# Kernel optimization log

Measured on AMD Instinct MI355X. Metric: run time of the kernel, lower is better.

Reference implementation:

```python
import jax, jax.numpy as jnp
import numpy as np

HEADS = 16
DIM_HEAD = 64
LN_EPS = 1e-5
COS_EPS = 1e-8


def setup_inputs() -> dict:
    key = jax.random.key(0)
    ks = jax.random.split(key, 5)
    dim = 1024
    inner = HEADS * DIM_HEAD
    q = jax.random.normal(ks[0], (4, 1024, dim), dtype=jnp.float32)
    k = jax.random.normal(ks[1], (4, 2048, dim), dtype=jnp.float32)
    v = jax.random.normal(ks[2], (4, 2048, dim), dtype=jnp.float32)
    W_in = jax.random.normal(ks[3], (dim, inner), dtype=jnp.float32) * (1.0 / np.sqrt(dim))
    W_out = jax.random.normal(ks[4], (inner, dim), dtype=jnp.float32) * (1.0 / np.sqrt(inner))
    ln_gamma = jnp.ones((dim,), dtype=jnp.float32)
    ln_beta = jnp.zeros((dim,), dtype=jnp.float32)
    b_out = jnp.zeros((dim,), dtype=jnp.float32)
    return {"q": q, "k": k, "v": v, "ln_gamma": ln_gamma, "ln_beta": ln_beta,
            "W_in": W_in, "W_out": W_out, "b_out": b_out}


def _layernorm(x, gamma, beta):
    mu = jnp.mean(x, axis=-1, keepdims=True)
    var = jnp.mean(jnp.square(x - mu), axis=-1, keepdims=True)  # biased, as torch
    return (x - mu) * jax.lax.rsqrt(var + LN_EPS) * gamma + beta


def _project(t, gamma, beta, W_in):
    # LayerNorm -> Linear(no bias) -> split heads: b n (h d) -> b h n d
    x = _layernorm(t, gamma, beta) @ W_in
    b, n, _ = x.shape
    return x.reshape(b, n, HEADS, DIM_HEAD).transpose(0, 2, 1, 3)


def reference(q, k, v, ln_gamma, ln_beta, W_in, W_out, b_out):
    f_q = _project(q, ln_gamma, ln_beta, W_in)  # [b,h,n,d]
    f_k = _project(k, ln_gamma, ln_beta, W_in)  # [b,h,m,d]
    f_v = _project(v, ln_gamma, ln_beta, W_in)  # [b,h,m,d]
    dots = jnp.einsum('bhnd,bhmd->bhnm', f_q, f_k)
    qn = jnp.linalg.norm(f_q, axis=-1, keepdims=True)          # [b,h,n,1]
    kn = jnp.linalg.norm(f_k, axis=-1, keepdims=True)          # [b,h,m,1]
    attn = dots / (qn * kn.transpose(0, 1, 3, 2) + COS_EPS)    # [b,h,n,m]
    out = jnp.einsum('bhnm,bhmd->bhnd', attn, f_v)             # [b,h,n,d]
    b, h, n, d = out.shape
    out = out.transpose(0, 2, 1, 3).reshape(b, n, h * d)       # b n (h d)
    return out @ W_out + b_out
```

## Files before the change

### kernel.cpp

```cpp
#include <hip/hip_runtime.h>

constexpr int BATCH = 4;
constexpr int SEQQ  = 1024;
constexpr int SEQK  = 2048;
constexpr int DIM   = 1024;
constexpr int NH    = 16;
constexpr int DH    = 64;
constexpr int RQ    = BATCH * SEQQ;
constexpr int RK    = BATCH * SEQK;
constexpr int RTOT  = RQ + 2 * RK;
constexpr int BH    = BATCH * NH;
constexpr int NSLC  = 8;
constexpr float LN_EPS = 1e-5f;

typedef _Float16 f16;
typedef __attribute__((ext_vector_type(8))) _Float16 f16x8;
typedef __attribute__((ext_vector_type(4))) float f32x4;

__device__ __forceinline__ void async16(const void* g, void* l) {
  __builtin_amdgcn_global_load_lds(
      (const __attribute__((address_space(1))) void*)g,
      (__attribute__((address_space(3))) void*)l, 16, 0, 0);
}

__global__ void __launch_bounds__(256) ln_to_f16(
    const float* __restrict__ q, const float* __restrict__ k,
    const float* __restrict__ v, const float* __restrict__ gamma,
    const float* __restrict__ beta, f16* __restrict__ a_h) {
  const int row = blockIdx.x * 4 + (threadIdx.x >> 6);
  const int lane = threadIdx.x & 63;
  const float* src;
  if (row < RQ)            src = q + (size_t)row * DIM;
  else if (row < RQ + RK)  src = k + (size_t)(row - RQ) * DIM;
  else                     src = v + (size_t)(row - RQ - RK) * DIM;
  float4 x[4];
  float s = 0.f, s2 = 0.f;
#pragma unroll
  for (int c = 0; c < 4; c++) {
    x[c] = ((const float4*)src)[c * 64 + lane];
    s  += x[c].x + x[c].y + x[c].z + x[c].w;
    s2 += x[c].x * x[c].x + x[c].y * x[c].y + x[c].z * x[c].z + x[c].w * x[c].w;
  }
#pragma unroll
  for (int off = 1; off < 64; off <<= 1) {
    s  += __shfl_xor(s, off);
    s2 += __shfl_xor(s2, off);
  }
  const float mu = s / DIM;
  const float rs = rsqrtf(s2 / DIM - mu * mu + LN_EPS);
#pragma unroll
  for (int c = 0; c < 4; c++) {
    float4 g = ((const float4*)gamma)[c * 64 + lane];
    float4 b = ((const float4*)beta)[c * 64 + lane];
    union { f16 h[4]; uint2 u; } o;
    o.h[0] = (f16)((x[c].x - mu) * rs * g.x + b.x);
    o.h[1] = (f16)((x[c].y - mu) * rs * g.y + b.y);
    o.h[2] = (f16)((x[c].z - mu) * rs * g.z + b.z);
    o.h[3] = (f16)((x[c].w - mu) * rs * g.w + b.w);
    ((uint2*)(a_h + (size_t)row * DIM))[c * 64 + lane] = o.u;
  }
}

__global__ void __launch_bounds__(256) transpose_f16(
    const float* __restrict__ W0, const float* __restrict__ W1,
    f16* __restrict__ T0, f16* __restrict__ T1) {
  const float* W = blockIdx.z ? W1 : W0;
  f16* T = blockIdx.z ? T1 : T0;
  __shared__ float tile[32][33];
  int tx = threadIdx.x & 31, ty = threadIdx.x >> 5;
  int k0 = blockIdx.x * 32, n0 = blockIdx.y * 32;
#pragma unroll
  for (int i = 0; i < 4; i++)
    tile[ty + 8 * i][tx] = W[(size_t)(k0 + ty + 8 * i) * DIM + n0 + tx];
  __syncthreads();
#pragma unroll
  for (int i = 0; i < 4; i++)
    T[(size_t)(n0 + ty + 8 * i) * DIM + k0 + tx] = (f16)tile[tx][ty + 8 * i];
}

template <int MT, bool OUT_F16, bool NORMS, bool BIAS, bool PERB>
__global__ void __launch_bounds__(256) mfma_gemm(
    const f16* __restrict__ A, const f16* __restrict__ Bt,
    void* __restrict__ Cout, const float* __restrict__ bias) {
  constexpr int JT = (MT == 128) ? 4 : 2;
  __shared__ f16 As[2][MT * 32];
  __shared__ f16 Bs[2][128 * 32];
  const int t = threadIdx.x;
  const int wid = t >> 6;
  const int lane = t & 63;
  const int row0 = blockIdx.x * MT;
  const int col0 = blockIdx.y * 128;
  const int wm = (MT == 128) ? (wid >> 1) * 64 : 0;
  const int wn = (MT == 128) ? (wid & 1) * 64 : wid * 32;

  const f16* BtB = PERB ? Bt + (size_t)(row0 >> 10) * DIM * DIM : Bt;

  const int rB = 32 * wid + (lane >> 2);
  const int qB = ((lane & 3) - ((rB >> 1) & 3)) & 3;
  const f16* gB = BtB + (size_t)(col0 + rB) * DIM + qB * 8;
  f16* lB0 = Bs[0] + 32 * wid * 32;
  f16* lB1 = Bs[1] + 32 * wid * 32;
  const int rA = (MT == 128 ? 32 : 16) * wid + (lane >> 2);
  const int qA = ((lane & 3) - ((rA >> 1) & 3)) & 3;
  const f16* gA = A + (size_t)(row0 + rA) * DIM + qA * 8;
  f16* lA0 = As[0] + (MT == 128 ? 32 : 16) * wid * 32;
  f16* lA1 = As[1] + (MT == 128 ? 32 : 16) * wid * 32;

  f32x4 acc[4][JT];
#pragma unroll
  for (int i = 0; i < 4; i++)
#pragma unroll
    for (int j = 0; j < JT; j++) acc[i][j] = (f32x4){0.f, 0.f, 0.f, 0.f};

  const int mrow = lane & 15;
  const int kq_p = (((lane >> 4) + ((lane >> 1) & 3)) & 3) * 8;

  for (int kt = 0; kt < DIM / 64; ++kt) {
    if (kt) __syncthreads();
    const int ko = kt * 64;
    async16(gA + ko,      lA0);
    if (MT == 128) async16(gA + ko + 16 * DIM, lA0 + 512);
    async16(gB + ko,      lB0);
    async16(gB + ko + 16 * DIM, lB0 + 512);
    async16(gA + ko + 32, lA1);
    if (MT == 128) async16(gA + ko + 32 + 16 * DIM, lA1 + 512);
    async16(gB + ko + 32, lB1);
    async16(gB + ko + 32 + 16 * DIM, lB1 + 512);
    __syncthreads();

#pragma unroll
    for (int h = 0; h < 2; ++h) {
      f16x8 af[4], bf[JT];
#pragma unroll
      for (int i = 0; i < 4; i++)
        af[i] = *(const f16x8*)(As[h] + (wm + i * 16 + mrow) * 32 + kq_p);
#pragma unroll
      for (int j = 0; j < JT; j++)
        bf[j] = *(const f16x8*)(Bs[h] + (wn + j * 16 + mrow) * 32 + kq_p);
#pragma unroll
      for (int i = 0; i < 4; i++)
#pragma unroll
        for (int j = 0; j < JT; j++)
          acc[i][j] = __builtin_amdgcn_mfma_f32_16x16x32_f16(af[i], bf[j], acc[i][j], 0, 0, 0);
    }
  }

  if (NORMS && MT == 128) {
    if (row0 < RQ + RK) {
      float sums[4][4];
#pragma unroll
      for (int i = 0; i < 4; i++)
#pragma unroll
        for (int r = 0; r < 4; r++) {
          float s = 0.f;
#pragma unroll
          for (int j = 0; j < JT; j++) s += acc[i][j][r] * acc[i][j][r];
          sums[i][r] = s;
        }
#pragma unroll
      for (int off = 1; off < 16; off <<= 1)
#pragma unroll
        for (int i = 0; i < 4; i++)
#pragma unroll
          for (int r = 0; r < 4; r++)
            sums[i][r] += __shfl_xor(sums[i][r], off);
#pragma unroll
      for (int i = 0; i < 4; i++)
#pragma unroll
        for (int r = 0; r < 4; r++) {
          const float inv = rsqrtf(sums[i][r]);
#pragma unroll
          for (int j = 0; j < JT; j++) acc[i][j][r] *= inv;
        }
    }
  }

  const int ccol = lane & 15;
  const int crow = (lane >> 4) * 4;
  if (OUT_F16) {
    f16* C = (f16*)Cout;
#pragma unroll
    for (int j = 0; j < JT; j++) {
      const int col = col0 + wn + j * 16 + ccol;
#pragma unroll
      for (int i = 0; i < 4; i++) {
        f16* Cp = C + (size_t)(row0 + wm + i * 16 + crow) * DIM + col;
#pragma unroll
        for (int r = 0; r < 4; r++) Cp[(size_t)r * DIM] = (f16)acc[i][j][r];
      }
    }
  } else {
    float* C = (float*)Cout;
#pragma unroll
    for (int j = 0; j < JT; j++) {
      const int col = col0 + wn + j * 16 + ccol;
      float bv = BIAS ? bias[col] : 0.f;
#pragma unroll
      for (int i = 0; i < 4; i++) {
        float* Cp = C + (size_t)(row0 + wm + i * 16 + crow) * DIM + col;
#pragma unroll
        for (int r = 0; r < 4; r++) Cp[(size_t)r * DIM] = acc[i][j][r] + bv;
      }
    }
  }
}

__global__ void __launch_bounds__(256) s_kernel(
    const f16* __restrict__ f, float* __restrict__ S4) {
  const int bh = blockIdx.x;
  const int b = bh >> 4, h = bh & 15;
  const int mbase = blockIdx.y * (SEQK / NSLC);
  const int t = threadIdx.x;
  __shared__ float ks[32][68];
  __shared__ float vs[32][68];
  const int lm   = t >> 3;
  const int lseg = (t & 7) * 8;
  const int d1 = (t & 15) * 4;
  const int d2 = (t >> 4) * 4;
  float acc[4][4] = {{0.f}};
  const f16* fk_base = f + ((size_t)RQ + (size_t)b * SEQK) * DIM + h * DH;
  const f16* fv_base = f + ((size_t)RQ + RK + (size_t)b * SEQK) * DIM + h * DH;

  int m = mbase + lm;
  f16x8 kv = *(const f16x8*)(fk_base + (size_t)m * DIM + lseg);
  f16x8 vv = *(const f16x8*)(fv_base + (size_t)m * DIM + lseg);

  constexpr int SUBS = SEQK / NSLC / 32;
  for (int sub = 0; sub < SUBS; ++sub) {
    __syncthreads();
#pragma unroll
    for (int e = 0; e < 8; e++) {
      ks[lm][lseg + e] = (float)kv[e];
      vs[lm][lseg + e] = (float)vv[e];
    }
    __syncthreads();
    if (sub + 1 < SUBS) {
      m = mbase + (sub + 1) * 32 + lm;
      kv = *(const f16x8*)(fk_base + (size_t)m * DIM + lseg);
      vv = *(const f16x8*)(fv_base + (size_t)m * DIM + lseg);
    }
#pragma unroll
    for (int mm = 0; mm < 32; ++mm) {
      float4 kk = *(const float4*)&ks[mm][d1];
      float4 vv2 = *(const float4*)&vs[mm][d2];
      acc[0][0] = fmaf(kk.x, vv2.x, acc[0][0]);
      acc[0][1] = fmaf(kk.x, vv2.y, acc[0][1]);
      acc[0][2] = fmaf(kk.x, vv2.z, acc[0][2]);
      acc[0][3] = fmaf(kk.x, vv2.w, acc[0][3]);
      acc[1][0] = fmaf(kk.y, vv2.x, acc[1][0]);
      acc[1][1] = fmaf(kk.y, vv2.y, acc[1][1]);
      acc[1][2] = fmaf(kk.y, vv2.z, acc[1][2]);
      acc[1][3] = fmaf(kk.y, vv2.w, acc[1][3]);
      acc[2][0] = fmaf(kk.z, vv2.x, acc[2][0]);
      acc[2][1] = fmaf(kk.z, vv2.y, acc[2][1]);
      acc[2][2] = fmaf(kk.z, vv2.z, acc[2][2]);
      acc[2][3] = fmaf(kk.z, vv2.w, acc[2][3]);
      acc[3][0] = fmaf(kk.w, vv2.x, acc[3][0]);
      acc[3][1] = fmaf(kk.w, vv2.y, acc[3][1]);
      acc[3][2] = fmaf(kk.w, vv2.z, acc[3][2]);
      acc[3][3] = fmaf(kk.w, vv2.w, acc[3][3]);
    }
  }
  float* Sp = S4 + ((size_t)blockIdx.y * BH + bh) * DH * DH;
#pragma unroll
  for (int i = 0; i < 4; i++)
#pragma unroll
    for (int j = 0; j < 4; j++)
      Sp[(d1 + i) * DH + (d2 + j)] = acc[i][j];
}

__global__ void __launch_bounds__(256) s_reduce(
    const float* __restrict__ S4, f16* __restrict__ Sh) {
  const int bh = blockIdx.x;
  const int t = threadIdx.x;
  const size_t base = (size_t)bh * DH * DH + t * 16;
  constexpr size_t STR = (size_t)BH * DH * DH;
#pragma unroll
  for (int c = 0; c < 4; c++) {
    float4 s = {0.f, 0.f, 0.f, 0.f};
#pragma unroll
    for (int p = 0; p < NSLC; p++) {
      float4 sp = *(const float4*)(S4 + base + p * STR + 4 * c);
      s.x += sp.x; s.y += sp.y; s.z += sp.z; s.w += sp.w;
    }
    union { f16 h[4]; uint2 u; } o;
    o.h[0] = (f16)s.x; o.h[1] = (f16)s.y; o.h[2] = (f16)s.z; o.h[3] = (f16)s.w;
    *(uint2*)(Sh + base + 4 * c) = o.u;
  }
}

__global__ void __launch_bounds__(256) m_build(
    const f16* __restrict__ wt_out, const f16* __restrict__ Sh,
    f16* __restrict__ Mt) {
  const int n0 = blockIdx.x * 128;
  const int bh = blockIdx.y;
  const int b = bh >> 4, h = bh & 15;
  __shared__ f16 As[128 * 64];
  __shared__ f16 Bs[64 * 64];
  const int t = threadIdx.x;
  const int wid = t >> 6, lane = t & 63;

  const f16* gA = wt_out + (size_t)(n0 + 32 * wid + (lane >> 3)) * DIM
                  + 64 * h + (lane & 7) * 8;
  f16* lA = As + 32 * wid * 64;
  const f16* gB = Sh + (size_t)bh * DH * DH + (16 * wid + (lane >> 3)) * 64
                  + (lane & 7) * 8;
  f16* lB = Bs + 16 * wid * 64;
#pragma unroll
  for (int o = 0; o < 4; o++) async16(gA + (size_t)(8 * o) * DIM, lA + 8 * o * 64);
  async16(gB, lB);
  async16(gB + 8 * 64, lB + 8 * 64);
  __syncthreads();

  const int wm = (wid >> 1) * 64;
  const int wn = (wid & 1) * 32;
  const int mrow = lane & 15;
  f32x4 acc[4][2];
#pragma unroll
  for (int i = 0; i < 4; i++)
#pragma unroll
    for (int j = 0; j < 2; j++) acc[i][j] = (f32x4){0.f, 0.f, 0.f, 0.f};

#pragma unroll
  for (int kh = 0; kh < 2; kh++) {
    const int kq = kh * 32 + (lane >> 4) * 8;
    f16x8 af[4], bf[2];
#pragma unroll
    for (int i = 0; i < 4; i++)
      af[i] = *(const f16x8*)(As + (wm + i * 16 + mrow) * 64 + kq);
#pragma unroll
    for (int j = 0; j < 2; j++)
      bf[j] = *(const f16x8*)(Bs + (wn + j * 16 + mrow) * 64 + kq);
#pragma unroll
    for (int i = 0; i < 4; i++)
#pragma unroll
      for (int j = 0; j < 2; j++)
        acc[i][j] = __builtin_amdgcn_mfma_f32_16x16x32_f16(af[i], bf[j], acc[i][j], 0, 0, 0);
  }

  const int ccol = lane & 15;
  const int crow = (lane >> 4) * 4;
  f16* Mb = Mt + (size_t)b * DIM * DIM;
#pragma unroll
  for (int j = 0; j < 2; j++) {
    const int col = 64 * h + wn + j * 16 + ccol;
#pragma unroll
    for (int i = 0; i < 4; i++) {
      f16* Mp = Mb + (size_t)(n0 + wm + i * 16 + crow) * DIM + col;
#pragma unroll
      for (int r = 0; r < 4; r++) Mp[(size_t)r * DIM] = (f16)acc[i][j][r];
    }
  }
}

extern "C" void kernel_launch(void* const* d_in, const int* in_sizes, int n_in,
                              void* d_out, int out_size, void* d_ws, size_t ws_size,
                              hipStream_t stream) {
  const float* q     = (const float*)d_in[0];
  const float* k     = (const float*)d_in[1];
  const float* v     = (const float*)d_in[2];
  const float* gamma = (const float*)d_in[3];
  const float* beta  = (const float*)d_in[4];
  const float* W_in  = (const float*)d_in[5];
  const float* W_out = (const float*)d_in[6];
  const float* b_out = (const float*)d_in[7];
  float* out = (float*)d_out;

  char* w = (char*)d_ws;
  f16*   f      = (f16*)w;
  f16*   a_h    = f + (size_t)RTOT * DIM;
  f16*   wt_in  = a_h + (size_t)RTOT * DIM;
  f16*   wt_out = wt_in + (size_t)DIM * DIM;
  f16*   Mt     = wt_out + (size_t)DIM * DIM;
  f16*   Sh     = Mt + (size_t)BATCH * DIM * DIM;
  float* S4     = (float*)(Sh + (size_t)BH * DH * DH);

  ln_to_f16<<<RTOT / 4, 256, 0, stream>>>(q, k, v, gamma, beta, a_h);
  transpose_f16<<<dim3(DIM / 32, DIM / 32, 2), 256, 0, stream>>>(
      W_in, W_out, wt_in, wt_out);

  mfma_gemm<128, true, true, false, false>
      <<<dim3(RTOT / 128, DIM / 128), 256, 0, stream>>>(a_h, wt_in, f, nullptr);

  s_kernel<<<dim3(BH, NSLC), 256, 0, stream>>>(f, S4);

  s_reduce<<<BH, 256, 0, stream>>>(S4, Sh);

  m_build<<<dim3(DIM / 128, BH), 256, 0, stream>>>(wt_out, Sh, Mt);

  mfma_gemm<64, false, false, true, true>
      <<<dim3(RQ / 64, DIM / 128), 256, 0, stream>>>(f, Mt, out, b_out);
}
```

Measured before the change: 240.4 us.

## Replace projection GEMM with 256x256-tile, 8-wave, multi-stage pipelined MFMA kernel

```diff
diff --git a/kernel.cpp b/kernel.cpp
--- a/kernel.cpp
+++ b/kernel.cpp
@@ -78,13 +78,140 @@
     T[(size_t)(n0 + ty + 8 * i) * DIM + k0 + tx] = (f16)tile[tx][ty + 8 * i];
 }
 
+constexpr int NT_K = DIM / 64;
+constexpr int NI_K = NT_K / 2;
+
+#define STAGE(P, gp, kt, BUFC, h)                                         \
+  do {                                                                    \
+    if ((kt) < NT_K) {                                                    \
+      f16* dst_ = (P) + ((BUFC) * 2 + (h)) * 8192 + lbase;                \
+      const f16* s0_ = (gp) + (kt) * 64 + (h) * 32;                       \
+      async16(s0_, dst_);                                                 \
+      async16(s0_ + (size_t)128 * DIM, dst_ + 128 * 32);                  \
+    }                                                                     \
+  } while (0)
+
+#define PHASE(PB, PK, PM, READB, SP, SG, skt, sbuf, sh)                   \
+  {                                                                       \
+    _Pragma("unroll") for (int f_ = 0; f_ < 4; ++f_)                      \
+      af[f_] = *(const f16x8*)(aBase + ((PB)*2 + (PK)) * 8192 +           \
+                               ((PM)*64 + f_*16) * 32);                   \
+    if (READB) {                                                          \
+      _Pragma("unroll") for (int j_ = 0; j_ < 4; ++j_)                    \
+        bf[j_] = *(const f16x8*)(bBase + ((PB)*2 + (PK)) * 8192 +         \
+                                 (j_*16) * 32);                           \
+    }                                                                     \
+    STAGE(SP, SG, skt, sbuf, sh);                                         \
+    __builtin_amdgcn_sched_barrier(0);                                    \
+    asm volatile("s_waitcnt vmcnt(8)" ::: "memory");                      \
+    __builtin_amdgcn_s_barrier();                                         \
+    __builtin_amdgcn_sched_barrier(0);                                    \
+    asm volatile("s_waitcnt lgkmcnt(0)" ::: "memory");                    \
+    __builtin_amdgcn_sched_barrier(0);                                    \
+    __builtin_amdgcn_s_setprio(1);                                        \
+    _Pragma("unroll") for (int f_ = 0; f_ < 4; ++f_)                      \
+      _Pragma("unroll") for (int j_ = 0; j_ < 4; ++j_)                    \
+        acc[(PM)*4 + f_][j_] = __builtin_amdgcn_mfma_f32_16x16x32_f16(    \
+            af[f_], bf[j_], acc[(PM)*4 + f_][j_], 0, 0, 0);               \
+    __builtin_amdgcn_s_setprio(0);                                        \
+    __builtin_amdgcn_sched_barrier(0);                                    \
+    __builtin_amdgcn_s_barrier();                                         \
+  }
+
+__global__ void __launch_bounds__(512, 2) proj_gemm(
+    const f16* __restrict__ A, const f16* __restrict__ Bt,
+    f16* __restrict__ C) {
+  __shared__ __align__(16) f16 As[2 * 2 * 256 * 32];
+  __shared__ __align__(16) f16 Bs[2 * 2 * 256 * 32];
+
+  const int t = threadIdx.x;
+  const int wid = t >> 6;
+  const int lane = t & 63;
+  const int la15 = lane & 15;
+
+  const int bid = blockIdx.x;
+  const int swz = (bid & 7) * 40 + (bid >> 3);
+  const int row0 = (swz >> 2) * 256;
+  const int col0 = (swz & 3) * 256;
+
+  const int wm = (wid >> 2) * 128;
+  const int wn = (wid & 3) * 64;
+
+  const size_t goff = (size_t)(wid * 16 + (lane >> 2)) * DIM +
+                      (((lane & 3) ^ ((lane >> 3) & 3)) * 8);
+  const f16* gA = A + (size_t)row0 * DIM + goff;
+  const f16* gB = Bt + (size_t)col0 * DIM + goff;
+  const int lbase = (wid * 16) * 32;
+
+  const int kslot = ((lane >> 4) ^ ((lane >> 1) & 3)) * 8;
+  const f16* aBase = As + (wm + la15) * 32 + kslot;
+  const f16* bBase = Bs + (wn + la15) * 32 + kslot;
+
+  f32x4 acc[8][4];
+#pragma unroll
+  for (int i = 0; i < 8; i++)
+#pragma unroll
+    for (int j = 0; j < 4; j++) acc[i][j] = (f32x4){0.f, 0.f, 0.f, 0.f};
+  f16x8 af[4], bf[4];
+
+  STAGE(As, gA, 0, 0, 0); STAGE(Bs, gB, 0, 0, 0);
+  STAGE(As, gA, 0, 0, 1); STAGE(Bs, gB, 0, 0, 1);
+  STAGE(As, gA, 1, 1, 0); STAGE(Bs, gB, 1, 1, 0);
+  __builtin_amdgcn_sched_barrier(0);
+  asm volatile("s_waitcnt vmcnt(8)" ::: "memory");
+  __builtin_amdgcn_s_barrier();
+  __builtin_amdgcn_sched_barrier(0);
+
+#pragma unroll 1
+  for (int it = 0; it < NI_K; ++it) {
+    const int t1 = 2 * it + 1, t2 = 2 * it + 2, t3 = 2 * it + 3;
+    PHASE(0, 0, 0, 1, As, gA, t1, 1, 1)
+    PHASE(0, 0, 1, 0, Bs, gB, t1, 1, 1)
+    PHASE(0, 1, 0, 1, As, gA, t2, 0, 0)
+    PHASE(0, 1, 1, 0, Bs, gB, t2, 0, 0)
+    PHASE(1, 0, 0, 1, As, gA, t2, 0, 1)
+    PHASE(1, 0, 1, 0, Bs, gB, t2, 0, 1)
+    PHASE(1, 1, 0, 1, As, gA, t3, 1, 0)
+    PHASE(1, 1, 1, 0, Bs, gB, t3, 1, 0)
+  }
+
+  if (row0 < RQ + RK) {
+#pragma unroll
+    for (int m = 0; m < 8; ++m)
+#pragma unroll
+      for (int r = 0; r < 4; ++r) {
+        float s = acc[m][0][r] * acc[m][0][r] + acc[m][1][r] * acc[m][1][r]
+                + acc[m][2][r] * acc[m][2][r] + acc[m][3][r] * acc[m][3][r];
+        s += __shfl_xor(s, 1);
+        s += __shfl_xor(s, 2);
+        s += __shfl_xor(s, 4);
+        s += __shfl_xor(s, 8);
+        const float inv = rsqrtf(s);
+#pragma unroll
+        for (int j = 0; j < 4; ++j) acc[m][j][r] *= inv;
+      }
+  }
+
+  const int crow = (lane >> 4) * 4;
+#pragma unroll
+  for (int j = 0; j < 4; ++j) {
+    const int col = col0 + wn + j * 16 + la15;
+#pragma unroll
+    for (int m = 0; m < 8; ++m) {
+      f16* Cp = C + (size_t)(row0 + wm + m * 16 + crow) * DIM + col;
+#pragma unroll
+      for (int r = 0; r < 4; ++r) Cp[(size_t)r * DIM] = (f16)acc[m][j][r];
+    }
+  }
+}
+
 template <int MT, bool OUT_F16, bool NORMS, bool BIAS, bool PERB>
 __global__ void __launch_bounds__(256) mfma_gemm(
     const f16* __restrict__ A, const f16* __restrict__ Bt,
     void* __restrict__ Cout, const float* __restrict__ bias) {
   constexpr int JT = (MT == 128) ? 4 : 2;
-  __shared__ f16 As[2][MT * 32];
-  __shared__ f16 Bs[2][128 * 32];
+  __shared__ f16 Asl[2][MT * 32];
+  __shared__ f16 Bsl[2][128 * 32];
   const int t = threadIdx.x;
   const int wid = t >> 6;
   const int lane = t & 63;
@@ -98,13 +225,13 @@
   const int rB = 32 * wid + (lane >> 2);
   const int qB = ((lane & 3) - ((rB >> 1) & 3)) & 3;
   const f16* gB = BtB + (size_t)(col0 + rB) * DIM + qB * 8;
-  f16* lB0 = Bs[0] + 32 * wid * 32;
-  f16* lB1 = Bs[1] + 32 * wid * 32;
+  f16* lB0 = Bsl[0] + 32 * wid * 32;
+  f16* lB1 = Bsl[1] + 32 * wid * 32;
   const int rA = (MT == 128 ? 32 : 16) * wid + (lane >> 2);
   const int qA = ((lane & 3) - ((rA >> 1) & 3)) & 3;
   const f16* gA = A + (size_t)(row0 + rA) * DIM + qA * 8;
-  f16* lA0 = As[0] + (MT == 128 ? 32 : 16) * wid * 32;
-  f16* lA1 = As[1] + (MT == 128 ? 32 : 16) * wid * 32;
+  f16* lA0 = Asl[0] + (MT == 128 ? 32 : 16) * wid * 32;
+  f16* lA1 = Asl[1] + (MT == 128 ? 32 : 16) * wid * 32;
 
   f32x4 acc[4][JT];
 #pragma unroll
@@ -133,10 +260,10 @@
       f16x8 af[4], bf[JT];
 #pragma unroll
       for (int i = 0; i < 4; i++)
-        af[i] = *(const f16x8*)(As[h] + (wm + i * 16 + mrow) * 32 + kq_p);
+        af[i] = *(const f16x8*)(Asl[h] + (wm + i * 16 + mrow) * 32 + kq_p);
 #pragma unroll
       for (int j = 0; j < JT; j++)
-        bf[j] = *(const f16x8*)(Bs[h] + (wn + j * 16 + mrow) * 32 + kq_p);
+        bf[j] = *(const f16x8*)(Bsl[h] + (wn + j * 16 + mrow) * 32 + kq_p);
 #pragma unroll
       for (int i = 0; i < 4; i++)
 #pragma unroll
@@ -295,17 +422,17 @@
   const int n0 = blockIdx.x * 128;
   const int bh = blockIdx.y;
   const int b = bh >> 4, h = bh & 15;
-  __shared__ f16 As[128 * 64];
-  __shared__ f16 Bs[64 * 64];
+  __shared__ f16 Asl[128 * 64];
+  __shared__ f16 Bsl[64 * 64];
   const int t = threadIdx.x;
   const int wid = t >> 6, lane = t & 63;
 
   const f16* gA = wt_out + (size_t)(n0 + 32 * wid + (lane >> 3)) * DIM
                   + 64 * h + (lane & 7) * 8;
-  f16* lA = As + 32 * wid * 64;
+  f16* lA = Asl + 32 * wid * 64;
   const f16* gB = Sh + (size_t)bh * DH * DH + (16 * wid + (lane >> 3)) * 64
                   + (lane & 7) * 8;
-  f16* lB = Bs + 16 * wid * 64;
+  f16* lB = Bsl + 16 * wid * 64;
 #pragma unroll
   for (int o = 0; o < 4; o++) async16(gA + (size_t)(8 * o) * DIM, lA + 8 * o * 64);
   async16(gB, lB);
@@ -327,10 +454,10 @@
     f16x8 af[4], bf[2];
 #pragma unroll
     for (int i = 0; i < 4; i++)
-      af[i] = *(const f16x8*)(As + (wm + i * 16 + mrow) * 64 + kq);
+      af[i] = *(const f16x8*)(Asl + (wm + i * 16 + mrow) * 64 + kq);
 #pragma unroll
     for (int j = 0; j < 2; j++)
-      bf[j] = *(const f16x8*)(Bs + (wn + j * 16 + mrow) * 64 + kq);
+      bf[j] = *(const f16x8*)(Bsl + (wn + j * 16 + mrow) * 64 + kq);
 #pragma unroll
     for (int i = 0; i < 4; i++)
 #pragma unroll
@@ -379,8 +506,7 @@
   transpose_f16<<<dim3(DIM / 32, DIM / 32, 2), 256, 0, stream>>>(
       W_in, W_out, wt_in, wt_out);
 
-  mfma_gemm<128, true, true, false, false>
-      <<<dim3(RTOT / 128, DIM / 128), 256, 0, stream>>>(a_h, wt_in, f, nullptr);
+  proj_gemm<<<dim3((RTOT / 256) * (DIM / 256)), 512, 0, stream>>>(a_h, wt_in, f);
 
   s_kernel<<<dim3(BH, NSLC), 256, 0, stream>>>(f, S4);
 
```

Measured after the change: 249.7 us. +3.9%, slower.

## Replace projection GEMM with large-tile 8-wave pipelined MFMA kernel

Applied to the files above, without the earlier changes.

```diff
diff --git a/kernel.cpp b/kernel.cpp
--- a/kernel.cpp
+++ b/kernel.cpp
@@ -78,13 +78,170 @@
     T[(size_t)(n0 + ty + 8 * i) * DIM + k0 + tx] = (f16)tile[tx][ty + 8 * i];
 }
 
+constexpr int PT_A = 320 * 64;
+constexpr int PT_B = 256 * 64;
+
+#define STAGE_A(buf, kt) do {                                        \
+    const f16* s_ = gA + (size_t)(kt) * 64;                          \
+    f16* d_ = AsW + (buf) * PT_A;                                    \
+    async16(s_,          d_);                                        \
+    async16(s_ +  65536, d_ + 4096);                                 \
+    async16(s_ + 131072, d_ + 8192);                                 \
+    async16(s_ + 196608, d_ + 12288);                                \
+    async16(s_ + 262144, d_ + 16384);                                \
+  } while (0)
+
+#define STAGE_B(buf, kt) do {                                        \
+    const f16* s_ = gB + (size_t)(kt) * 64;                          \
+    f16* d_ = BsW + (buf) * PT_B;                                    \
+    async16(s_,          d_);                                        \
+    async16(s_ +  65536, d_ + 4096);                                 \
+    async16(s_ + 131072, d_ + 8192);                                 \
+    async16(s_ + 196608, d_ + 12288);                                \
+  } while (0)
+
+#define WT5 asm volatile("s_waitcnt vmcnt(5)" ::: "memory")
+#define WT0 asm volatile("s_waitcnt vmcnt(0)" ::: "memory")
+#define WTN ((void)0)
+#define STN ((void)0)
+
+#define PH(BUF, H, MH, RB, STG, WT) {                                \
+    STG;                                                             \
+    __builtin_amdgcn_sched_barrier(0);                               \
+    WT;                                                              \
+    __builtin_amdgcn_s_barrier();                                    \
+    __builtin_amdgcn_sched_barrier(0);                               \
+    if (RB) {                                                        \
+      _Pragma("unroll") for (int j_ = 0; j_ < 4; ++j_)               \
+        bf[j_] = *(const f16x8*)(bB##H + (BUF) * PT_B + j_ * 1024);  \
+    }                                                                \
+    _Pragma("unroll") for (int f_ = 0; f_ < 5; ++f_)                 \
+      af[f_] = *(const f16x8*)(aB##H + (BUF) * PT_A + (MH) * 5120 +  \
+                               f_ * 1024);                           \
+    __builtin_amdgcn_s_setprio(1);                                   \
+    _Pragma("unroll") for (int f_ = 0; f_ < 5; ++f_)                 \
+      _Pragma("unroll") for (int j_ = 0; j_ < 4; ++j_)               \
+        acc[(MH) * 5 + f_][j_] = __builtin_amdgcn_mfma_f32_16x16x32_f16( \
+            af[f_], bf[j_], acc[(MH) * 5 + f_][j_], 0, 0, 0);        \
+    __builtin_amdgcn_s_setprio(0);                                   \
+    __builtin_amdgcn_sched_barrier(0);                               \
+    __builtin_amdgcn_s_barrier();                                    \
+  }
+
+__global__ void __launch_bounds__(512, 2) proj_gemm(
+    const f16* __restrict__ A, const f16* __restrict__ Bt,
+    f16* __restrict__ C) {
+  __shared__ __align__(16) f16 As[2 * PT_A];
+  __shared__ __align__(16) f16 Bs[2 * PT_B];
+
+  const int tid = threadIdx.x;
+  const int wid = tid >> 6;
+  const int lane = tid & 63;
+  const int la15 = lane & 15;
+
+  const int bid = blockIdx.x;
+  const int swz = (bid & 7) * 32 + (bid >> 3);
+  const int row0 = (swz >> 2) * 320;
+  const int col0 = (swz & 3) * 256;
+
+  const int wm = (wid >> 2) * 160;
+  const int wn = (wid & 3) * 64;
+
+  const int hs = (tid & 7) ^ ((tid >> 3) & 7);
+  const f16* gA = A + (size_t)(row0 + (tid >> 3)) * DIM + (hs >> 2) * 32 +
+                  (hs & 3) * 8;
+  const f16* gB = Bt + (size_t)(col0 + (tid >> 3)) * DIM + (hs >> 2) * 32 +
+                  (hs & 3) * 8;
+  f16* AsW = As + wid * 512;
+  f16* BsW = Bs + wid * 512;
+
+  const int g = lane >> 4;
+  const int r7 = la15 & 7;
+  const int cs0 = (g ^ r7) * 8;
+  const int cs1 = ((4 + g) ^ r7) * 8;
+  const f16* aB0 = As + (wm + la15) * 64 + cs0;
+  const f16* aB1 = As + (wm + la15) * 64 + cs1;
+  const f16* bB0 = Bs + (wn + la15) * 64 + cs0;
+  const f16* bB1 = Bs + (wn + la15) * 64 + cs1;
+
+  f32x4 acc[10][4];
+#pragma unroll
+  for (int i = 0; i < 10; i++)
+#pragma unroll
+    for (int j = 0; j < 4; j++) acc[i][j] = (f32x4){0.f, 0.f, 0.f, 0.f};
+  f16x8 af[5], bf[4];
+
+  STAGE_A(0, 0);
+  STAGE_B(0, 0);
+  __builtin_amdgcn_sched_barrier(0);
+  WT0;
+  __builtin_amdgcn_s_barrier();
+  __builtin_amdgcn_sched_barrier(0);
+
+#pragma unroll 1
+  for (int it = 0; it < 7; ++it) {
+    const int t1 = 2 * it + 1, t2 = 2 * it + 2;
+    PH(0, 0, 0, 1, STAGE_A(1, t1), WT5)
+    PH(0, 0, 1, 0, STAGE_B(1, t1), WTN)
+    PH(0, 1, 0, 1, STN,            WTN)
+    PH(0, 1, 1, 0, STN,            WTN)
+    PH(1, 0, 0, 1, STAGE_A(0, t2), WT5)
+    PH(1, 0, 1, 0, STAGE_B(0, t2), WTN)
+    PH(1, 1, 0, 1, STN,            WTN)
+    PH(1, 1, 1, 0, STN,            WTN)
+  }
+  PH(0, 0, 0, 1, STAGE_A(1, 15), WT5)
+  PH(0, 0, 1, 0, STAGE_B(1, 15), WTN)
+  PH(0, 1, 0, 1, STN,            WTN)
+  PH(0, 1, 1, 0, STN,            WTN)
+  PH(1, 0, 0, 1, STN,            WT0)
+  PH(1, 0, 1, 0, STN,            WTN)
+  PH(1, 1, 0, 1, STN,            WTN)
+  PH(1, 1, 1, 0, STN,            WTN)
+
+  const int crow = (lane >> 4) * 4;
+#pragma unroll
+  for (int mh = 0; mh < 2; ++mh)
+#pragma unroll
+    for (int f = 0; f < 5; ++f) {
+      const int m = mh * 5 + f;
+      const int rbase = row0 + wm + mh * 80 + f * 16 + crow;
+#pragma unroll
+      for (int r = 0; r < 4; ++r) {
+        float s = acc[m][0][r] * acc[m][0][r] + acc[m][1][r] * acc[m][1][r]
+                + acc[m][2][r] * acc[m][2][r] + acc[m][3][r] * acc[m][3][r];
+        s += __shfl_xor(s, 1);
+        s += __shfl_xor(s, 2);
+        s += __shfl_xor(s, 4);
+        s += __shfl_xor(s, 8);
+        if (rbase + r < RQ + RK) {
+          const float inv = rsqrtf(s);
+#pragma unroll
+          for (int j = 0; j < 4; ++j) acc[m][j][r] *= inv;
+        }
+      }
+    }
+
+#pragma unroll
+  for (int j = 0; j < 4; ++j) {
+    const int col = col0 + wn + j * 16 + la15;
+#pragma unroll
+    for (int m = 0; m < 10; ++m) {
+      const int rb = row0 + wm + (m / 5) * 80 + (m % 5) * 16 + crow;
+      f16* Cp = C + (size_t)rb * DIM + col;
+#pragma unroll
+      for (int r = 0; r < 4; ++r) Cp[(size_t)r * DIM] = (f16)acc[m][j][r];
+    }
+  }
+}
+
 template <int MT, bool OUT_F16, bool NORMS, bool BIAS, bool PERB>
 __global__ void __launch_bounds__(256) mfma_gemm(
     const f16* __restrict__ A, const f16* __restrict__ Bt,
     void* __restrict__ Cout, const float* __restrict__ bias) {
   constexpr int JT = (MT == 128) ? 4 : 2;
-  __shared__ f16 As[2][MT * 32];
-  __shared__ f16 Bs[2][128 * 32];
+  __shared__ f16 Asl[2][MT * 32];
+  __shared__ f16 Bsl[2][128 * 32];
   const int t = threadIdx.x;
   const int wid = t >> 6;
   const int lane = t & 63;
@@ -98,13 +255,13 @@
   const int rB = 32 * wid + (lane >> 2);
   const int qB = ((lane & 3) - ((rB >> 1) & 3)) & 3;
   const f16* gB = BtB + (size_t)(col0 + rB) * DIM + qB * 8;
-  f16* lB0 = Bs[0] + 32 * wid * 32;
-  f16* lB1 = Bs[1] + 32 * wid * 32;
+  f16* lB0 = Bsl[0] + 32 * wid * 32;
+  f16* lB1 = Bsl[1] + 32 * wid * 32;
   const int rA = (MT == 128 ? 32 : 16) * wid + (lane >> 2);
   const int qA = ((lane & 3) - ((rA >> 1) & 3)) & 3;
   const f16* gA = A + (size_t)(row0 + rA) * DIM + qA * 8;
-  f16* lA0 = As[0] + (MT == 128 ? 32 : 16) * wid * 32;
-  f16* lA1 = As[1] + (MT == 128 ? 32 : 16) * wid * 32;
+  f16* lA0 = Asl[0] + (MT == 128 ? 32 : 16) * wid * 32;
+  f16* lA1 = Asl[1] + (MT == 128 ? 32 : 16) * wid * 32;
 
   f32x4 acc[4][JT];
 #pragma unroll
@@ -133,10 +290,10 @@
       f16x8 af[4], bf[JT];
 #pragma unroll
       for (int i = 0; i < 4; i++)
-        af[i] = *(const f16x8*)(As[h] + (wm + i * 16 + mrow) * 32 + kq_p);
+        af[i] = *(const f16x8*)(Asl[h] + (wm + i * 16 + mrow) * 32 + kq_p);
 #pragma unroll
       for (int j = 0; j < JT; j++)
-        bf[j] = *(const f16x8*)(Bs[h] + (wn + j * 16 + mrow) * 32 + kq_p);
+        bf[j] = *(const f16x8*)(Bsl[h] + (wn + j * 16 + mrow) * 32 + kq_p);
 #pragma unroll
       for (int i = 0; i < 4; i++)
 #pragma unroll
@@ -295,17 +452,17 @@
   const int n0 = blockIdx.x * 128;
   const int bh = blockIdx.y;
   const int b = bh >> 4, h = bh & 15;
-  __shared__ f16 As[128 * 64];
-  __shared__ f16 Bs[64 * 64];
+  __shared__ f16 Asl[128 * 64];
+  __shared__ f16 Bsl[64 * 64];
   const int t = threadIdx.x;
   const int wid = t >> 6, lane = t & 63;
 
   const f16* gA = wt_out + (size_t)(n0 + 32 * wid + (lane >> 3)) * DIM
                   + 64 * h + (lane & 7) * 8;
-  f16* lA = As + 32 * wid * 64;
+  f16* lA = Asl + 32 * wid * 64;
   const f16* gB = Sh + (size_t)bh * DH * DH + (16 * wid + (lane >> 3)) * 64
                   + (lane & 7) * 8;
-  f16* lB = Bs + 16 * wid * 64;
+  f16* lB = Bsl + 16 * wid * 64;
 #pragma unroll
   for (int o = 0; o < 4; o++) async16(gA + (size_t)(8 * o) * DIM, lA + 8 * o * 64);
   async16(gB, lB);
@@ -327,10 +484,10 @@
     f16x8 af[4], bf[2];
 #pragma unroll
     for (int i = 0; i < 4; i++)
-      af[i] = *(const f16x8*)(As + (wm + i * 16 + mrow) * 64 + kq);
+      af[i] = *(const f16x8*)(Asl + (wm + i * 16 + mrow) * 64 + kq);
 #pragma unroll
     for (int j = 0; j < 2; j++)
-      bf[j] = *(const f16x8*)(Bs + (wn + j * 16 + mrow) * 64 + kq);
+      bf[j] = *(const f16x8*)(Bsl + (wn + j * 16 + mrow) * 64 + kq);
 #pragma unroll
     for (int i = 0; i < 4; i++)
 #pragma unroll
@@ -379,8 +536,7 @@
   transpose_f16<<<dim3(DIM / 32, DIM / 32, 2), 256, 0, stream>>>(
       W_in, W_out, wt_in, wt_out);
 
-  mfma_gemm<128, true, true, false, false>
-      <<<dim3(RTOT / 128, DIM / 128), 256, 0, stream>>>(a_h, wt_in, f, nullptr);
+  proj_gemm<<<dim3(256), 512, 0, stream>>>(a_h, wt_in, f);
 
   s_kernel<<<dim3(BH, NSLC), 256, 0, stream>>>(f, S4);
 
```

Measured after the change: 238.9 us. No clear change (-0.6%).
